# Kernel optimization log

Hardware: AMD Instinct MI355X
Metric: run time of the kernel (lower is better)

The kernel has to match this reference:

```python
import jax, jax.numpy as jnp
import numpy as np

H = 4096      # hidden_size
Hk = 16       # num_key_heads
Dk = 256      # key_head_dim
Hv = 32       # num_value_heads
Dv = 256      # value_head_dim
G = 2         # kv_group_size
Ve = 512      # value_expand = G*Dv
CS = 4        # conv_size
QK = Hk * Dk  # 4096
VD = Hv * Dv  # 8192
EPS = 1e-6


def setup_inputs() -> dict:
    key = jax.random.key(0)
    ks = jax.random.split(key, 14)
    n = lambda i, shape, s: jax.random.normal(ks[i], shape, jnp.float32) * s
    return {
        "hidden_states": n(0, (1, H, 1, 1), 1.0),
        "Wq": n(1, (QK, H), 0.02),
        "Wk": n(2, (QK, H), 0.02),
        "Wv": n(3, (VD, H), 0.02),
        "Wo": n(4, (H, VD), 0.02),
        "Wa": n(5, (Hk, H), 0.02),
        "Wb": n(6, (Hk, H), 0.02),
        "q_conv_w": n(7, (1, QK, CS), 0.5),
        "k_conv_w": n(8, (1, QK, CS), 0.5),
        "v_conv_w": n(9, (1, VD, CS), 0.5),
        "q_cache": n(10, (1, QK, CS - 1), 1.0),
        "k_cache": n(11, (1, QK, CS - 1), 1.0),
        "v_cache": n(12, (1, VD, CS - 1), 1.0),
        "state": n(13, (1, Hk, Dk, Ve), 0.1),
    }


def _l2norm(x):
    return x * jax.lax.rsqrt(jnp.sum(x * x, axis=-1, keepdims=True) + EPS)


def reference(hidden_states, Wq, Wk, Wv, Wo, Wa, Wb,
              q_conv_w, k_conv_w, v_conv_w,
              q_cache, k_cache, v_cache, state):
    h = hidden_states[0, :, 0, 0]  # [H]
    q = Wq @ h                      # [QK]
    k = Wk @ h                      # [QK]
    v = Wv @ h                      # [VD]
    alpha = jax.nn.sigmoid(Wa @ h)  # [Hk]
    beta = jax.nn.sigmoid(Wb @ h)   # [Hk]

    # depthwise causal conv via cache concat + mul-sum, then SiLU
    q_full = jnp.concatenate([q_cache, q[None, :, None]], axis=2)  # [1,QK,CS]
    k_full = jnp.concatenate([k_cache, k[None, :, None]], axis=2)
    v_full = jnp.concatenate([v_cache, v[None, :, None]], axis=2)  # [1,VD,CS]
    q1 = jax.nn.silu(jnp.sum(q_full * q_conv_w, axis=2))  # [1,QK]
    k1 = jax.nn.silu(jnp.sum(k_full * k_conv_w, axis=2))
    v1 = jax.nn.silu(jnp.sum(v_full * v_conv_w, axis=2))  # [1,VD]

    q_heads = _l2norm(q1.reshape(1, Hk, Dk))
    k_heads = _l2norm(k1.reshape(1, Hk, Dk))
    v_heads = v1.reshape(1, Hk, Ve)  # Hv=Hk*G, Ve=G*Dv

    a = alpha.reshape(1, Hk, 1, 1)
    b = beta.reshape(1, Hk, 1, 1)
    state_decayed = state * a                                   # [1,Hk,Dk,Ve]
    retrieved = jnp.einsum('bhdv,bhd->bhv', state_decayed, k_heads)
    error = v_heads - retrieved                                 # [1,Hk,Ve]
    outer = k_heads[..., None] * error[:, :, None, :]           # [1,Hk,Dk,Ve]
    new_state = state_decayed + b * outer
    out = jnp.einsum('bhdv,bhd->bhv', new_state, q_heads)       # [1,Hk,Ve]
    out = out.reshape(1, VD)
    output = (out @ Wo.T).reshape(1, H, 1, 1)
    return output
```

## Files before the change

### kernel.cpp

```cpp
#include <hip/hip_runtime.h>
#include <math.h>

#define HDIM 4096
#define HK 16
#define DK 256
#define VE 512
#define QK 4096
#define VD 8192
#define NCHUNK 16
#define DPC 16
#define EPS 1e-6f

#define OFF_Q    0
#define OFF_K    4096
#define OFF_V    8192
#define OFF_AB   16384
#define OFF_SIG  16416
#define OFF_QH   16448
#define OFF_KH   20544
#define OFF_VH   24640
#define OFF_KQ   32832
#define OFF_OUT  32848
#define OFF_PQ   41040
#define OFF_PK   (41040 + NCHUNK*VD)

__device__ __forceinline__ float sigmoidf_(float x) { return 1.f / (1.f + __expf(-x)); }
__device__ __forceinline__ float siluf_(float x)    { return x / (1.f + __expf(-x)); }

__global__ __launch_bounds__(256) void k1_gemv_all(
    const float* __restrict__ hvec,
    const float* __restrict__ Wq, const float* __restrict__ Wk,
    const float* __restrict__ Wv, const float* __restrict__ Wa,
    const float* __restrict__ Wb, float* __restrict__ ws) {
  int wave = threadIdx.x >> 6;
  int lane = threadIdx.x & 63;
  int row = blockIdx.x * 4 + wave;
  if (row >= 16416) return;

  const float* W; float* out; int r;
  if (row < 4096)        { W = Wq; r = row;         out = ws + OFF_Q; }
  else if (row < 8192)   { W = Wk; r = row - 4096;  out = ws + OFF_K; }
  else if (row < 16384)  { W = Wv; r = row - 8192;  out = ws + OFF_V; }
  else if (row < 16400)  { W = Wa; r = row - 16384; out = ws + OFF_AB; }
  else                   { W = Wb; r = row - 16400; out = ws + OFF_AB + 16; }

  const float4* row4 = (const float4*)(W + (size_t)r * HDIM);
  const float4* h4   = (const float4*)hvec;
  float acc = 0.f;
#pragma unroll
  for (int j = 0; j < 16; ++j) {
    float4 w = row4[j * 64 + lane];
    float4 hv = h4[j * 64 + lane];
    acc += w.x * hv.x + w.y * hv.y + w.z * hv.z + w.w * hv.w;
  }
#pragma unroll
  for (int off = 32; off; off >>= 1) acc += __shfl_xor(acc, off, 64);
  if (lane == 0) out[r] = acc;
}

__global__ __launch_bounds__(256) void k2_conv_norm(
    const float* __restrict__ qcw, const float* __restrict__ kcw,
    const float* __restrict__ vcw,
    const float* __restrict__ qc,  const float* __restrict__ kc,
    const float* __restrict__ vc,  float* __restrict__ ws) {
  int hh = blockIdx.x;
  int d  = threadIdx.x;
  int i  = hh * DK + d;

  float q1 = qc[i*3+0]*qcw[i*4+0] + qc[i*3+1]*qcw[i*4+1] + qc[i*3+2]*qcw[i*4+2]
           + ws[OFF_Q + i]*qcw[i*4+3];
  q1 = siluf_(q1);
  float k1 = kc[i*3+0]*kcw[i*4+0] + kc[i*3+1]*kcw[i*4+1] + kc[i*3+2]*kcw[i*4+2]
           + ws[OFF_K + i]*kcw[i*4+3];
  k1 = siluf_(k1);

  int iv0 = hh * VE + d, iv1 = iv0 + 256;
  float v0 = vc[iv0*3+0]*vcw[iv0*4+0] + vc[iv0*3+1]*vcw[iv0*4+1] + vc[iv0*3+2]*vcw[iv0*4+2]
           + ws[OFF_V + iv0]*vcw[iv0*4+3];
  float v1 = vc[iv1*3+0]*vcw[iv1*4+0] + vc[iv1*3+1]*vcw[iv1*4+1] + vc[iv1*3+2]*vcw[iv1*4+2]
           + ws[OFF_V + iv1]*vcw[iv1*4+3];
  ws[OFF_VH + iv0] = siluf_(v0);
  ws[OFF_VH + iv1] = siluf_(v1);

  float a = q1 * q1, b = k1 * k1, c = q1 * k1;
#pragma unroll
  for (int off = 32; off; off >>= 1) {
    a += __shfl_xor(a, off, 64);
    b += __shfl_xor(b, off, 64);
    c += __shfl_xor(c, off, 64);
  }
  __shared__ float sA[4], sB[4], sC[4];
  int wave = threadIdx.x >> 6, lane = threadIdx.x & 63;
  if (lane == 0) { sA[wave] = a; sB[wave] = b; sC[wave] = c; }
  __syncthreads();
  float ssq = sA[0] + sA[1] + sA[2] + sA[3];
  float ssk = sB[0] + sB[1] + sB[2] + sB[3];
  float sqk = sC[0] + sC[1] + sC[2] + sC[3];
  float rq = rsqrtf(ssq + EPS), rk = rsqrtf(ssk + EPS);

  ws[OFF_QH + i] = q1 * rq;
  ws[OFF_KH + i] = k1 * rk;
  if (d == 0) ws[OFF_KQ + hh] = sqk * rq * rk;
  if (hh == 0 && d < 32) ws[OFF_SIG + d] = sigmoidf_(ws[OFF_AB + d]);
}

__global__ __launch_bounds__(512) void k3_state_partial(
    const float* __restrict__ state, float* __restrict__ ws) {
  int hh = blockIdx.x >> 4;
  int c  = blockIdx.x & 15;
  int vv = threadIdx.x;
  int d0 = c * DPC;
  float aq = 0.f, ak = 0.f;
#pragma unroll
  for (int t = 0; t < DPC; ++t) {
    int d = d0 + t;
    float s = state[((size_t)(hh * DK + d)) * VE + vv];
    aq += s * ws[OFF_QH + hh * DK + d];
    ak += s * ws[OFF_KH + hh * DK + d];
  }
  ws[OFF_PQ + c * VD + hh * VE + vv] = aq;
  ws[OFF_PK + c * VD + hh * VE + vv] = ak;
}

__global__ __launch_bounds__(512) void k4_combine(float* __restrict__ ws) {
  int hh = blockIdx.x, vv = threadIdx.x;
  float Sq = 0.f, Sk = 0.f;
#pragma unroll
  for (int c = 0; c < NCHUNK; ++c) {
    Sq += ws[OFF_PQ + c * VD + hh * VE + vv];
    Sk += ws[OFF_PK + c * VD + hh * VE + vv];
  }
  float a  = ws[OFF_SIG + hh];
  float b  = ws[OFF_SIG + 16 + hh];
  float kq = ws[OFF_KQ + hh];
  float vh = ws[OFF_VH + hh * VE + vv];
  ws[OFF_OUT + hh * VE + vv] = a * Sq + b * kq * (vh - a * Sk);
}

__global__ __launch_bounds__(256) void k5_gemv_out(
    const float* __restrict__ Wo, const float* __restrict__ ws,
    float* __restrict__ dout) {
  int wave = threadIdx.x >> 6;
  int lane = threadIdx.x & 63;
  int row = blockIdx.x * 4 + wave;
  const float4* row4 = (const float4*)(Wo + (size_t)row * VD);
  const float4* o4   = (const float4*)(ws + OFF_OUT);
  float acc = 0.f;
#pragma unroll
  for (int j = 0; j < 32; ++j) {
    float4 w = row4[j * 64 + lane];
    float4 o = o4[j * 64 + lane];
    acc += w.x * o.x + w.y * o.y + w.z * o.z + w.w * o.w;
  }
#pragma unroll
  for (int off = 32; off; off >>= 1) acc += __shfl_xor(acc, off, 64);
  if (lane == 0) dout[row] = acc;
}

extern "C" void kernel_launch(void* const* d_in, const int* in_sizes, int n_in,
                              void* d_out, int out_size, void* d_ws, size_t ws_size,
                              hipStream_t stream) {
  const float* hvec = (const float*)d_in[0];
  const float* Wq   = (const float*)d_in[1];
  const float* Wk   = (const float*)d_in[2];
  const float* Wv   = (const float*)d_in[3];
  const float* Wo   = (const float*)d_in[4];
  const float* Wa   = (const float*)d_in[5];
  const float* Wb   = (const float*)d_in[6];
  const float* qcw  = (const float*)d_in[7];
  const float* kcw  = (const float*)d_in[8];
  const float* vcw  = (const float*)d_in[9];
  const float* qc   = (const float*)d_in[10];
  const float* kc   = (const float*)d_in[11];
  const float* vc   = (const float*)d_in[12];
  const float* state= (const float*)d_in[13];
  float* ws  = (float*)d_ws;
  float* out = (float*)d_out;

  k1_gemv_all<<<4104, 256, 0, stream>>>(hvec, Wq, Wk, Wv, Wa, Wb, ws);
  k2_conv_norm<<<16, 256, 0, stream>>>(qcw, kcw, vcw, qc, kc, vc, ws);
  k3_state_partial<<<256, 512, 0, stream>>>(state, ws);
  k4_combine<<<16, 512, 0, stream>>>(ws);
  k5_gemv_out<<<1024, 256, 0, stream>>>(Wo, ws, out);
}
```

Before: 81.63 us.

## Fuse conv/norm into state kernel, v-conv into combine; two rows per wave in GEMVs

Removes the separate conv/normalization kernel. Each state-partial block now recomputes the q/k conv, SiLU and L2-norm for its head in shared memory. The v conv and the alpha/beta sigmoids move into the combine kernel, and the normalization scales are applied to the partial sums after accumulation. Both GEMV kernels now stage the input vector in LDS and have each wave process two rows, halving the grid. This saves one launch and some global round-trips, at the cost of sixteen redundant conv/norm computations per head.

```diff
diff --git a/kernel.cpp b/kernel.cpp
--- a/kernel.cpp
+++ b/kernel.cpp
@@ -15,146 +15,164 @@
 #define OFF_K    4096
 #define OFF_V    8192
 #define OFF_AB   16384
-#define OFF_SIG  16416
-#define OFF_QH   16448
-#define OFF_KH   20544
-#define OFF_VH   24640
-#define OFF_KQ   32832
-#define OFF_OUT  32848
-#define OFF_PQ   41040
-#define OFF_PK   (41040 + NCHUNK*VD)
+#define OFF_KQ   16416
+#define OFF_OUT  16432
+#define OFF_PQ   24624
+#define OFF_PK   (24624 + NCHUNK*VD)
 
 __device__ __forceinline__ float sigmoidf_(float x) { return 1.f / (1.f + __expf(-x)); }
 __device__ __forceinline__ float siluf_(float x)    { return x / (1.f + __expf(-x)); }
 
-__global__ __launch_bounds__(256) void k1_gemv_all(
+__device__ __forceinline__ void resolve_row(
+    int row, const float* Wq, const float* Wk, const float* Wv,
+    const float* Wa, const float* Wb, float* ws,
+    const float4** w4, float** outp) {
+  if (row < 4096)       { *w4 = (const float4*)(Wq + (size_t)row * HDIM);            *outp = ws + OFF_Q + row; }
+  else if (row < 8192)  { int r = row - 4096;  *w4 = (const float4*)(Wk + (size_t)r * HDIM); *outp = ws + OFF_K + r; }
+  else if (row < 16384) { int r = row - 8192;  *w4 = (const float4*)(Wv + (size_t)r * HDIM); *outp = ws + OFF_V + r; }
+  else if (row < 16400) { int r = row - 16384; *w4 = (const float4*)(Wa + (size_t)r * HDIM); *outp = ws + OFF_AB + r; }
+  else                  { int r = row - 16400; *w4 = (const float4*)(Wb + (size_t)r * HDIM); *outp = ws + OFF_AB + 16 + r; }
+}
+
+__global__ __launch_bounds__(256, 4) void k1_gemv_all(
     const float* __restrict__ hvec,
     const float* __restrict__ Wq, const float* __restrict__ Wk,
     const float* __restrict__ Wv, const float* __restrict__ Wa,
     const float* __restrict__ Wb, float* __restrict__ ws) {
-  int wave = threadIdx.x >> 6;
-  int lane = threadIdx.x & 63;
-  int row = blockIdx.x * 4 + wave;
-  if (row >= 16416) return;
-
-  const float* W; float* out; int r;
-  if (row < 4096)        { W = Wq; r = row;         out = ws + OFF_Q; }
-  else if (row < 8192)   { W = Wk; r = row - 4096;  out = ws + OFF_K; }
-  else if (row < 16384)  { W = Wv; r = row - 8192;  out = ws + OFF_V; }
-  else if (row < 16400)  { W = Wa; r = row - 16384; out = ws + OFF_AB; }
-  else                   { W = Wb; r = row - 16400; out = ws + OFF_AB + 16; }
-
-  const float4* row4 = (const float4*)(W + (size_t)r * HDIM);
-  const float4* h4   = (const float4*)hvec;
-  float acc = 0.f;
+  __shared__ float4 hs4[1024];
+  int tid = threadIdx.x;
+  const float4* h4 = (const float4*)hvec;
+#pragma unroll
+  for (int k = 0; k < 4; ++k) hs4[tid + k * 256] = h4[tid + k * 256];
+  __syncthreads();
+
+  int wave = tid >> 6, lane = tid & 63;
+  int row0 = blockIdx.x * 8 + wave * 2;
+
+  const float4 *w4a, *w4b; float *oa, *ob;
+  resolve_row(row0,     Wq, Wk, Wv, Wa, Wb, ws, &w4a, &oa);
+  resolve_row(row0 + 1, Wq, Wk, Wv, Wa, Wb, ws, &w4b, &ob);
+
+  float acc0 = 0.f, acc1 = 0.f;
 #pragma unroll
   for (int j = 0; j < 16; ++j) {
-    float4 w = row4[j * 64 + lane];
-    float4 hv = h4[j * 64 + lane];
-    acc += w.x * hv.x + w.y * hv.y + w.z * hv.z + w.w * hv.w;
-  }
-#pragma unroll
-  for (int off = 32; off; off >>= 1) acc += __shfl_xor(acc, off, 64);
-  if (lane == 0) out[r] = acc;
-}
-
-__global__ __launch_bounds__(256) void k2_conv_norm(
+    float4 w0 = w4a[j * 64 + lane];
+    float4 w1 = w4b[j * 64 + lane];
+    float4 hv = hs4[j * 64 + lane];
+    acc0 += w0.x * hv.x + w0.y * hv.y + w0.z * hv.z + w0.w * hv.w;
+    acc1 += w1.x * hv.x + w1.y * hv.y + w1.z * hv.z + w1.w * hv.w;
+  }
+#pragma unroll
+  for (int off = 32; off; off >>= 1) {
+    acc0 += __shfl_xor(acc0, off, 64);
+    acc1 += __shfl_xor(acc1, off, 64);
+  }
+  if (lane == 0) { *oa = acc0; *ob = acc1; }
+}
+
+__global__ __launch_bounds__(512) void kB_state(
     const float* __restrict__ qcw, const float* __restrict__ kcw,
-    const float* __restrict__ vcw,
     const float* __restrict__ qc,  const float* __restrict__ kc,
-    const float* __restrict__ vc,  float* __restrict__ ws) {
-  int hh = blockIdx.x;
-  int d  = threadIdx.x;
-  int i  = hh * DK + d;
-
-  float q1 = qc[i*3+0]*qcw[i*4+0] + qc[i*3+1]*qcw[i*4+1] + qc[i*3+2]*qcw[i*4+2]
-           + ws[OFF_Q + i]*qcw[i*4+3];
-  q1 = siluf_(q1);
-  float k1 = kc[i*3+0]*kcw[i*4+0] + kc[i*3+1]*kcw[i*4+1] + kc[i*3+2]*kcw[i*4+2]
-           + ws[OFF_K + i]*kcw[i*4+3];
-  k1 = siluf_(k1);
-
-  int iv0 = hh * VE + d, iv1 = iv0 + 256;
-  float v0 = vc[iv0*3+0]*vcw[iv0*4+0] + vc[iv0*3+1]*vcw[iv0*4+1] + vc[iv0*3+2]*vcw[iv0*4+2]
-           + ws[OFF_V + iv0]*vcw[iv0*4+3];
-  float v1 = vc[iv1*3+0]*vcw[iv1*4+0] + vc[iv1*3+1]*vcw[iv1*4+1] + vc[iv1*3+2]*vcw[iv1*4+2]
-           + ws[OFF_V + iv1]*vcw[iv1*4+3];
-  ws[OFF_VH + iv0] = siluf_(v0);
-  ws[OFF_VH + iv1] = siluf_(v1);
-
-  float a = q1 * q1, b = k1 * k1, c = q1 * k1;
-#pragma unroll
-  for (int off = 32; off; off >>= 1) {
-    a += __shfl_xor(a, off, 64);
-    b += __shfl_xor(b, off, 64);
-    c += __shfl_xor(c, off, 64);
-  }
-  __shared__ float sA[4], sB[4], sC[4];
-  int wave = threadIdx.x >> 6, lane = threadIdx.x & 63;
-  if (lane == 0) { sA[wave] = a; sB[wave] = b; sC[wave] = c; }
-  __syncthreads();
-  float ssq = sA[0] + sA[1] + sA[2] + sA[3];
-  float ssk = sB[0] + sB[1] + sB[2] + sB[3];
-  float sqk = sC[0] + sC[1] + sC[2] + sC[3];
-  float rq = rsqrtf(ssq + EPS), rk = rsqrtf(ssk + EPS);
-
-  ws[OFF_QH + i] = q1 * rq;
-  ws[OFF_KH + i] = k1 * rk;
-  if (d == 0) ws[OFF_KQ + hh] = sqk * rq * rk;
-  if (hh == 0 && d < 32) ws[OFF_SIG + d] = sigmoidf_(ws[OFF_AB + d]);
-}
-
-__global__ __launch_bounds__(512) void k3_state_partial(
     const float* __restrict__ state, float* __restrict__ ws) {
   int hh = blockIdx.x >> 4;
   int c  = blockIdx.x & 15;
-  int vv = threadIdx.x;
+  int tid = threadIdx.x;
+  __shared__ float q1s[DK], k1s[DK];
+  __shared__ float red[3][8];
+
+  float a = 0.f, b = 0.f, cc = 0.f;
+  if (tid < DK) {
+    int i = hh * DK + tid;
+    float q1 = qc[i*3+0]*qcw[i*4+0] + qc[i*3+1]*qcw[i*4+1] + qc[i*3+2]*qcw[i*4+2]
+             + ws[OFF_Q + i]*qcw[i*4+3];
+    q1 = siluf_(q1);
+    float k1 = kc[i*3+0]*kcw[i*4+0] + kc[i*3+1]*kcw[i*4+1] + kc[i*3+2]*kcw[i*4+2]
+             + ws[OFF_K + i]*kcw[i*4+3];
+    k1 = siluf_(k1);
+    q1s[tid] = q1; k1s[tid] = k1;
+    a = q1 * q1; b = k1 * k1; cc = q1 * k1;
+  }
+#pragma unroll
+  for (int off = 32; off; off >>= 1) {
+    a  += __shfl_xor(a, off, 64);
+    b  += __shfl_xor(b, off, 64);
+    cc += __shfl_xor(cc, off, 64);
+  }
+  int wave = tid >> 6, lane = tid & 63;
+  if (lane == 0) { red[0][wave] = a; red[1][wave] = b; red[2][wave] = cc; }
+  __syncthreads();
+  float ssq = 0.f, ssk = 0.f, skq = 0.f;
+#pragma unroll
+  for (int w = 0; w < 8; ++w) { ssq += red[0][w]; ssk += red[1][w]; skq += red[2][w]; }
+  float rq = rsqrtf(ssq + EPS), rk = rsqrtf(ssk + EPS);
+  if (c == 0 && tid == 0) ws[OFF_KQ + hh] = skq * rq * rk;
+
+  int vv = tid;
   int d0 = c * DPC;
   float aq = 0.f, ak = 0.f;
 #pragma unroll
   for (int t = 0; t < DPC; ++t) {
     int d = d0 + t;
     float s = state[((size_t)(hh * DK + d)) * VE + vv];
-    aq += s * ws[OFF_QH + hh * DK + d];
-    ak += s * ws[OFF_KH + hh * DK + d];
-  }
-  ws[OFF_PQ + c * VD + hh * VE + vv] = aq;
-  ws[OFF_PK + c * VD + hh * VE + vv] = ak;
-}
-
-__global__ __launch_bounds__(512) void k4_combine(float* __restrict__ ws) {
-  int hh = blockIdx.x, vv = threadIdx.x;
+    aq += s * q1s[d];
+    ak += s * k1s[d];
+  }
+  ws[OFF_PQ + c * VD + hh * VE + vv] = aq * rq;
+  ws[OFF_PK + c * VD + hh * VE + vv] = ak * rk;
+}
+
+__global__ __launch_bounds__(128) void kC_combine(
+    const float* __restrict__ vcw, const float* __restrict__ vc,
+    float* __restrict__ ws) {
+  int hh = blockIdx.x >> 2;
+  int vv = (blockIdx.x & 3) * 128 + threadIdx.x;
+  int col = hh * VE + vv;
+
   float Sq = 0.f, Sk = 0.f;
 #pragma unroll
   for (int c = 0; c < NCHUNK; ++c) {
-    Sq += ws[OFF_PQ + c * VD + hh * VE + vv];
-    Sk += ws[OFF_PK + c * VD + hh * VE + vv];
-  }
-  float a  = ws[OFF_SIG + hh];
-  float b  = ws[OFF_SIG + 16 + hh];
+    Sq += ws[OFF_PQ + c * VD + col];
+    Sk += ws[OFF_PK + c * VD + col];
+  }
+  float v1 = vc[col*3+0]*vcw[col*4+0] + vc[col*3+1]*vcw[col*4+1] + vc[col*3+2]*vcw[col*4+2]
+           + ws[OFF_V + col]*vcw[col*4+3];
+  float vh = siluf_(v1);
+  float a  = sigmoidf_(ws[OFF_AB + hh]);
+  float bb = sigmoidf_(ws[OFF_AB + 16 + hh]);
   float kq = ws[OFF_KQ + hh];
-  float vh = ws[OFF_VH + hh * VE + vv];
-  ws[OFF_OUT + hh * VE + vv] = a * Sq + b * kq * (vh - a * Sk);
-}
-
-__global__ __launch_bounds__(256) void k5_gemv_out(
+  ws[OFF_OUT + col] = a * Sq + bb * kq * (vh - a * Sk);
+}
+
+__global__ __launch_bounds__(256, 4) void kD_gemv_out(
     const float* __restrict__ Wo, const float* __restrict__ ws,
     float* __restrict__ dout) {
-  int wave = threadIdx.x >> 6;
-  int lane = threadIdx.x & 63;
-  int row = blockIdx.x * 4 + wave;
-  const float4* row4 = (const float4*)(Wo + (size_t)row * VD);
-  const float4* o4   = (const float4*)(ws + OFF_OUT);
-  float acc = 0.f;
+  __shared__ float4 os4[2048];
+  int tid = threadIdx.x;
+  const float4* o4 = (const float4*)(ws + OFF_OUT);
+#pragma unroll
+  for (int k = 0; k < 8; ++k) os4[tid + k * 256] = o4[tid + k * 256];
+  __syncthreads();
+
+  int wave = tid >> 6, lane = tid & 63;
+  int row0 = blockIdx.x * 8 + wave * 2;
+  const float4* r0 = (const float4*)(Wo + (size_t)row0 * VD);
+  const float4* r1 = (const float4*)(Wo + (size_t)(row0 + 1) * VD);
+
+  float acc0 = 0.f, acc1 = 0.f;
 #pragma unroll
   for (int j = 0; j < 32; ++j) {
-    float4 w = row4[j * 64 + lane];
-    float4 o = o4[j * 64 + lane];
-    acc += w.x * o.x + w.y * o.y + w.z * o.z + w.w * o.w;
-  }
-#pragma unroll
-  for (int off = 32; off; off >>= 1) acc += __shfl_xor(acc, off, 64);
-  if (lane == 0) dout[row] = acc;
+    float4 w0 = r0[j * 64 + lane];
+    float4 w1 = r1[j * 64 + lane];
+    float4 ov = os4[j * 64 + lane];
+    acc0 += w0.x * ov.x + w0.y * ov.y + w0.z * ov.z + w0.w * ov.w;
+    acc1 += w1.x * ov.x + w1.y * ov.y + w1.z * ov.z + w1.w * ov.w;
+  }
+#pragma unroll
+  for (int off = 32; off; off >>= 1) {
+    acc0 += __shfl_xor(acc0, off, 64);
+    acc1 += __shfl_xor(acc1, off, 64);
+  }
+  if (lane == 0) { dout[row0] = acc0; dout[row0 + 1] = acc1; }
 }
 
 extern "C" void kernel_launch(void* const* d_in, const int* in_sizes, int n_in,
@@ -177,9 +195,8 @@
   float* ws  = (float*)d_ws;
   float* out = (float*)d_out;
 
-  k1_gemv_all<<<4104, 256, 0, stream>>>(hvec, Wq, Wk, Wv, Wa, Wb, ws);
-  k2_conv_norm<<<16, 256, 0, stream>>>(qcw, kcw, vcw, qc, kc, vc, ws);
-  k3_state_partial<<<256, 512, 0, stream>>>(state, ws);
-  k4_combine<<<16, 512, 0, stream>>>(ws);
-  k5_gemv_out<<<1024, 256, 0, stream>>>(Wo, ws, out);
-}
+  k1_gemv_all<<<2052, 256, 0, stream>>>(hvec, Wq, Wk, Wv, Wa, Wb, ws);
+  kB_state<<<256, 512, 0, stream>>>(qcw, kcw, qc, kc, state, ws);
+  kC_combine<<<64, 128, 0, stream>>>(vcw, vc, ws);
+  kD_gemv_out<<<512, 256, 0, stream>>>(Wo, ws, out);
+}
```

Measured after the change: 92.32 us. +13.1%, slower.
